# Kernel optimization log

Measured on AMD Instinct MI355X. Metric: run time of the kernel, lower is better.

Reference implementation:

```python
import jax, jax.numpy as jnp
from jax import lax
import numpy as np

ALPHA = 0.5
MAX_ITERS = 40
TOL = 1e-6
BITS = 8


def fake_quant_sym(w, bits=BITS):
    # symmetric per-tensor fake quantisation
    qmax = float(2 ** (bits - 1) - 1)
    scale = jnp.max(jnp.abs(w)) / qmax
    return jnp.round(w / scale) * scale


def fb_solve(Wq, Uq, bq, x, alpha=ALPHA, max_iters=MAX_ITERS, tol=TOL):
    # forward-backward splitting fixed-point solve: z = relu((1-a)z + a(Wz + Ux^T + b))
    n = Wq.shape[0]
    B = x.shape[0]
    Ux = Uq @ x.T + bq[:, None]  # (n, B), constant across iterations

    def cond(carry):
        z, res, it = carry
        return jnp.logical_and(it < max_iters, res >= tol)

    def body(carry):
        z, _, it = carry
        u = (1.0 - alpha) * z + alpha * (Wq @ z + Ux)
        z_next = jax.nn.relu(u)  # relu_prox
        res = jnp.linalg.norm(z_next - z) / (jnp.linalg.norm(z) + 1e-12)
        return z_next, res, it + 1

    z0 = jnp.zeros((n, B), dtype=x.dtype)
    z, _, _ = lax.while_loop(cond, body, (z0, jnp.array(jnp.inf, dtype=x.dtype), 0))
    u_star = (1.0 - alpha) * z + alpha * (Wq @ z + Ux)
    mask = (u_star > 0).astype(x.dtype)  # relu Jacobian mask D*
    return z, mask


def setup_inputs() -> dict:
    key = jax.random.key(0)
    k0, k1, k2, k3, k4 = jax.random.split(key, 5)
    n, d, B, C = 512, 784, 128, 10
    # scale W so ||W||_2 < 1 (monotone operator condition m > 0)
    W = 0.3 * jax.random.normal(k0, (n, n), dtype=jnp.float32) / jnp.sqrt(n)
    U = jax.random.normal(k1, (n, d), dtype=jnp.float32) / jnp.sqrt(d)
    b = 0.01 * jax.random.normal(k2, (n,), dtype=jnp.float32)
    x = jax.random.normal(k3, (B, d), dtype=jnp.float32)
    Wc = jax.random.normal(k4, (C, n), dtype=jnp.float32) / jnp.sqrt(n)
    bc = jnp.zeros((C,), dtype=jnp.float32)
    return {"W": W, "U": U, "b": b, "x": x, "Wc": Wc, "bc": bc}


def reference(W, U, b, x, Wc, bc):
    # post-training fake quantisation of W, U, b (done once at init in torch)
    Wq = fake_quant_sym(W)
    Uq = fake_quant_sym(U)
    bq = fake_quant_sym(b)
    z_star, _ = fb_solve(Wq, Uq, bq, x)  # (n, B)
    logits = z_star.T @ Wc.T + bc  # classifier on z*^T
    return logits
```

## Files before the change

### kernel.cpp

```cpp
#include <hip/hip_runtime.h>
#include <hip/hip_bf16.h>


#define N_DIM 512
#define D_DIM 784
#define B_DIM 128
#define C_DIM 10
#define QMAX 127.0f
#define N_ITERS 40
#define HILO_START 28
#define ZPITCH 528
#define UXPITCH 520
#define MT 4

typedef int    i32x4  __attribute__((ext_vector_type(4)));
typedef float  f32x4  __attribute__((ext_vector_type(4)));
typedef __bf16 bf16x8 __attribute__((ext_vector_type(8)));

__device__ __forceinline__ float pscale64(const float* __restrict__ p) {
    float m = 0.0f;
#pragma unroll 16
    for (int i = 0; i < 64; ++i) m = fmaxf(m, p[i]);
    return m * (1.0f / QMAX);
}

__global__ void maxabs_kernel(const float* __restrict__ W,
                              const float* __restrict__ U,
                              const float* __restrict__ b,
                              float* __restrict__ partials) {
    const float4* src;
    int n4;
    if (blockIdx.y == 0)      { src = (const float4*)W; n4 = N_DIM * N_DIM / 4; }
    else if (blockIdx.y == 1) { src = (const float4*)U; n4 = N_DIM * D_DIM / 4; }
    else                      { src = (const float4*)b; n4 = N_DIM / 4; }
    float m = 0.0f;
    for (int i = blockIdx.x * blockDim.x + threadIdx.x; i < n4; i += gridDim.x * blockDim.x) {
        float4 v = src[i];
        m = fmaxf(m, fmaxf(fmaxf(fabsf(v.x), fabsf(v.y)), fmaxf(fabsf(v.z), fabsf(v.w))));
    }
    __shared__ float red[256];
    red[threadIdx.x] = m;
    __syncthreads();
    for (int s = 128; s > 0; s >>= 1) {
        if (threadIdx.x < s) red[threadIdx.x] = fmaxf(red[threadIdx.x], red[threadIdx.x + s]);
        __syncthreads();
    }
    if (threadIdx.x == 0) partials[blockIdx.y * 64 + blockIdx.x] = red[0];
}

__global__ __launch_bounds__(256) void prep_kernel(const float* __restrict__ W,
                                                   const float* __restrict__ U,
                                                   const float* __restrict__ b,
                                                   const float* __restrict__ x,
                                                   const float* __restrict__ partials,
                                                   int* __restrict__ rowsum,
                                                   signed char* __restrict__ Qp8,
                                                   float* __restrict__ UxT) {
    const int t = threadIdx.x;
    if (blockIdx.x < 256) {
        __shared__ int ls[4];
        const float s = pscale64(partials);
        const float inv = 1.0f / s;
        int idx = blockIdx.x * 256 + t;
        float4 w = ((const float4*)W)[idx];
        int k = (idx << 2) & (N_DIM - 1);
        int r = (idx << 2) >> 9;
        int q0 = (int)rintf(w.x * inv);
        int q1 = (int)rintf(w.y * inv);
        int q2 = (int)rintf(w.z * inv);
        int q3 = (int)rintf(w.w * inv);
        char4 c;
        c.x = (signed char)q0; c.y = (signed char)q1;
        c.z = (signed char)q2; c.w = (signed char)q3;
        int kc = k >> 6, q = (k >> 4) & 3, jj = k & 15;
        *(char4*)&Qp8[((kc << 9) + r) * 64 + q * 16 + jj] = c;
        int psum = q0 + q1 + q2 + q3;
#pragma unroll
        for (int s2 = 1; s2 < 64; s2 <<= 1) psum += __shfl_xor(psum, s2);
        if ((t & 63) == 0) ls[t >> 6] = psum;
        __syncthreads();
        if (t == 0) {
            rowsum[2 * blockIdx.x]     = ls[0] + ls[1];
            rowsum[2 * blockIdx.x + 1] = ls[2] + ls[3];
        }
    } else {
        const float sU = pscale64(partials + 64);
        const float invU = 1.0f / sU;
        const float sb = pscale64(partials + 128);
        const int bx = blockIdx.x - 256;
        const int wave = t >> 6, lane = t & 63;
        const int m = lane & 15, quad = lane >> 4;
        const int i0 = (bx >> 3) * 64 + wave * 16;
        const int c0 = (bx & 7) * 16;
        const float* urow = U + (i0 + m) * D_DIM;
        const float* xrow = x + (c0 + m) * D_DIM;
        f32x4 acc = {};
#pragma unroll 4
        for (int kcc = 0; kcc < 24; ++kcc) {
            int kbase = kcc * 32 + (quad << 3);
            float4 u0 = *(const float4*)(urow + kbase);
            float4 u1 = *(const float4*)(urow + kbase + 4);
            float4 x0 = *(const float4*)(xrow + kbase);
            float4 x1 = *(const float4*)(xrow + kbase + 4);
            float uu[8] = {u0.x, u0.y, u0.z, u0.w, u1.x, u1.y, u1.z, u1.w};
            float xx[8] = {x0.x, x0.y, x0.z, x0.w, x1.x, x1.y, x1.z, x1.w};
            bf16x8 a, xh, xl;
#pragma unroll
            for (int j = 0; j < 8; ++j) {
                a[j] = (__bf16)rintf(uu[j] * invU);
                __bf16 h = (__bf16)xx[j];
                xh[j] = h;
                xl[j] = (__bf16)(xx[j] - (float)h);
            }
            acc = __builtin_amdgcn_mfma_f32_16x16x32_bf16(a, xh, acc, 0, 0, 0);
            acc = __builtin_amdgcn_mfma_f32_16x16x32_bf16(a, xl, acc, 0, 0, 0);
        }
        {
            bf16x8 a, xh, xl;
            if (quad < 2) {
                int kbase = 768 + (quad << 3);
                float4 u0 = *(const float4*)(urow + kbase);
                float4 u1 = *(const float4*)(urow + kbase + 4);
                float4 x0 = *(const float4*)(xrow + kbase);
                float4 x1 = *(const float4*)(xrow + kbase + 4);
                float uu[8] = {u0.x, u0.y, u0.z, u0.w, u1.x, u1.y, u1.z, u1.w};
                float xx[8] = {x0.x, x0.y, x0.z, x0.w, x1.x, x1.y, x1.z, x1.w};
#pragma unroll
                for (int j = 0; j < 8; ++j) {
                    a[j] = (__bf16)rintf(uu[j] * invU);
                    __bf16 h = (__bf16)xx[j];
                    xh[j] = h;
                    xl[j] = (__bf16)(xx[j] - (float)h);
                }
            } else {
#pragma unroll
                for (int j = 0; j < 8; ++j) {
                    a[j] = (__bf16)0.0f; xh[j] = (__bf16)0.0f; xl[j] = (__bf16)0.0f;
                }
            }
            acc = __builtin_amdgcn_mfma_f32_16x16x32_bf16(a, xh, acc, 0, 0, 0);
            acc = __builtin_amdgcn_mfma_f32_16x16x32_bf16(a, xl, acc, 0, 0, 0);
        }
        const int row0 = i0 + (quad << 2);
        f32x4 o;
#pragma unroll
        for (int r = 0; r < 4; ++r)
            o[r] = sU * acc[r] + rintf(b[row0 + r] / sb) * sb;
        *(f32x4*)&UxT[(c0 + m) * N_DIM + row0] = o;
    }
}

__global__ __launch_bounds__(512, 2) void solve_kernel(const signed char* __restrict__ Qp8,
                                                       const float* __restrict__ UxT,
                                                       const float* __restrict__ partials,
                                                       const int* __restrict__ rowsum,
                                                       const float* __restrict__ Wc,
                                                       const float* __restrict__ bc,
                                                       float* __restrict__ out) {
    __shared__ signed char zh[2][16][ZPITCH];
    __shared__ signed char zl[2][16][ZPITCH];
    __shared__ float UxS[16][UXPITCH];
    __shared__ float red[32][16][C_DIM];
    const int t = threadIdx.x;
    const int wave = t >> 6;
    const int lane = t & 63;
    const int m = lane & 15;
    const int quad = lane >> 4;
    const int c0 = blockIdx.x * 16;
    const float sW = pscale64(partials);
    const float c1 = sW * (1.0f / 2048.0f);

    for (int i = t; i < 16 * N_DIM; i += 512) {
        int c = i >> 9, r = i & (N_DIM - 1);
        float v = UxT[(c0 + c) * N_DIM + r];
        float z1 = fmaxf(0.5f * v, 0.0f);
        int vq = (int)rintf(z1 * 2048.0f);
        vq = min(vq, 32767);
        zh[0][c][r] = (signed char)(vq >> 8);
        zl[0][c][r] = (signed char)((vq & 255) - 128);
        UxS[c][r] = v + c1 * 128.0f * (float)rowsum[r];
    }

    const int rowbase = wave * 64;
    i32x4 A[MT][8];
#pragma unroll
    for (int ti = 0; ti < MT; ++ti)
#pragma unroll
        for (int kc = 0; kc < 8; ++kc)
            A[ti][kc] = *(const i32x4*)&Qp8[((kc << 9) + rowbase + ti * 16 + m) * 64 + (quad << 4)];
#pragma unroll
    for (int ti = 0; ti < MT; ++ti)
#pragma unroll
        for (int kc = 0; kc < 8; ++kc)
            asm volatile("" : "+v"(A[ti][kc]));
    __syncthreads();

    int cur = 0;
    for (int it = 1; it < N_ITERS; ++it) {
        const bool lo = (it >= HILO_START);
        i32x4 acch[MT] = {};
        i32x4 accl[MT] = {};
        if (lo) {
#pragma unroll
            for (int kc = 0; kc < 8; ++kc) {
                i32x4 bh = *(const i32x4*)&zh[cur][m][(kc << 6) + (quad << 4)];
                i32x4 bl = *(const i32x4*)&zl[cur][m][(kc << 6) + (quad << 4)];
#pragma unroll
                for (int ti = 0; ti < MT; ++ti) {
                    acch[ti] = __builtin_amdgcn_mfma_i32_16x16x64_i8(A[ti][kc], bh, acch[ti], 0, 0, 0);
                    accl[ti] = __builtin_amdgcn_mfma_i32_16x16x64_i8(A[ti][kc], bl, accl[ti], 0, 0, 0);
                }
            }
        } else {
#pragma unroll
            for (int kc = 0; kc < 8; ++kc) {
                i32x4 bh = *(const i32x4*)&zh[cur][m][(kc << 6) + (quad << 4)];
#pragma unroll
                for (int ti = 0; ti < MT; ++ti)
                    acch[ti] = __builtin_amdgcn_mfma_i32_16x16x64_i8(A[ti][kc], bh, acch[ti], 0, 0, 0);
            }
        }
        const int nxt = cur ^ 1;
#pragma unroll
        for (int ti = 0; ti < MT; ++ti) {
            const int row0 = rowbase + ti * 16 + (quad << 2);
            f32x4 uxv = *(const f32x4*)&UxS[m][row0];
            char4 ph = *(const char4*)&zh[cur][m][row0];
            char4 pl = *(const char4*)&zl[cur][m][row0];
            char4 nh, nl;
#pragma unroll
            for (int r = 0; r < 4; ++r) {
                int vp = (((int)((&ph.x)[r])) << 8) + (int)((&pl.x)[r]) + 128;
                int qv = (acch[ti][r] << 8) + (lo ? accl[ti][r] : 0);
                float u = 0.5f * ((float)vp * (1.0f / 2048.0f))
                        + 0.5f * (c1 * (float)qv + uxv[r]);
                float zn = fmaxf(u, 0.0f);
                int vq = (int)rintf(zn * 2048.0f);
                vq = min(vq, 32767);
                (&nh.x)[r] = (signed char)(vq >> 8);
                (&nl.x)[r] = (signed char)((vq & 255) - 128);
            }
            *(char4*)&zh[nxt][m][row0] = nh;
            *(char4*)&zl[nxt][m][row0] = nl;
        }
        __syncthreads();
        cur = nxt;
    }

    {
        const int seg = t >> 4;
        const int colL = t & 15;
        float p[C_DIM];
#pragma unroll
        for (int cl = 0; cl < C_DIM; ++cl) p[cl] = 0.0f;
        const int r0 = seg * 16;
#pragma unroll
        for (int rr = 0; rr < 16; ++rr) {
            int r = r0 + rr;
            int v = (((int)zh[cur][colL][r]) << 8) + (int)zl[cur][colL][r] + 128;
            float zv = (float)v * (1.0f / 2048.0f);
#pragma unroll
            for (int cl = 0; cl < C_DIM; ++cl)
                p[cl] += zv * Wc[cl * N_DIM + r];
        }
#pragma unroll
        for (int cl = 0; cl < C_DIM; ++cl) red[seg][colL][cl] = p[cl];
        __syncthreads();
        for (int s = 16; s > 0; s >>= 1) {
            if (seg < s) {
#pragma unroll
                for (int cl = 0; cl < C_DIM; ++cl)
                    red[seg][colL][cl] += red[seg + s][colL][cl];
            }
            __syncthreads();
        }
        if (t < 16 * C_DIM) {
            int col = t & 15;
            int cl  = t >> 4;
            out[(c0 + col) * C_DIM + cl] = red[0][col][cl] + bc[cl];
        }
    }
}

extern "C" void kernel_launch(void* const* d_in, const int* in_sizes, int n_in,
                              void* d_out, int out_size, void* d_ws, size_t ws_size,
                              hipStream_t stream) {
    const float* W  = (const float*)d_in[0];
    const float* U  = (const float*)d_in[1];
    const float* b  = (const float*)d_in[2];
    const float* x  = (const float*)d_in[3];
    const float* Wc = (const float*)d_in[4];
    const float* bc = (const float*)d_in[5];
    float* out = (float*)d_out;

    float* ws = (float*)d_ws;
    float* partials = ws;
    int* rowsum = (int*)(ws + 256);
    signed char* Qp8 = (signed char*)(ws + 256 + 512);
    float* UxT = ws + 256 + 512 + (N_DIM * N_DIM / 4);

    maxabs_kernel<<<dim3(64, 3), 256, 0, stream>>>(W, U, b, partials);
    prep_kernel<<<320, 256, 0, stream>>>(W, U, b, x, partials, rowsum, Qp8, UxT);
    solve_kernel<<<8, 512, 0, stream>>>(Qp8, UxT, partials, rowsum, Wc, bc, out);
}
```

Measured before the change: 166.1 us.

## Keep iterate z and Ux in registers; restage Ux GEMM through LDS

Result: faster. 158.3 us (-4.7%).

```diff
diff --git a/kernel.cpp b/kernel.cpp
--- a/kernel.cpp
+++ b/kernel.cpp
@@ -10,8 +10,8 @@
 #define N_ITERS 40
 #define HILO_START 28
 #define ZPITCH 528
-#define UXPITCH 520
 #define MT 4
+#define UPITCH 808
 
 typedef int    i32x4  __attribute__((ext_vector_type(4)));
 typedef float  f32x4  __attribute__((ext_vector_type(4)));
@@ -56,9 +56,13 @@
                                                    int* __restrict__ rowsum,
                                                    signed char* __restrict__ Qp8,
                                                    float* __restrict__ UxT) {
+    __shared__ __bf16 uS[16][UPITCH];
+    __shared__ __bf16 xhS[16][UPITCH];
+    __shared__ __bf16 xlS[16][UPITCH];
+    __shared__ f32x4  sacc[4][64];
+    __shared__ int ls[4];
     const int t = threadIdx.x;
     if (blockIdx.x < 256) {
-        __shared__ int ls[4];
         const float s = pscale64(partials);
         const float inv = 1.0f / s;
         int idx = blockIdx.x * 256 + t;
@@ -88,65 +92,46 @@
         const float invU = 1.0f / sU;
         const float sb = pscale64(partials + 128);
         const int bx = blockIdx.x - 256;
+        const int i0 = (bx >> 3) * 16;
+        const int c0 = (bx & 7) * 16;
+        for (int r = 0; r < 16; ++r) {
+            for (int k = t; k < D_DIM; k += 256) {
+                float uv = U[(i0 + r) * D_DIM + k];
+                uS[r][k] = (__bf16)rintf(uv * invU);
+                float xv = x[(c0 + r) * D_DIM + k];
+                __bf16 h = (__bf16)xv;
+                xhS[r][k] = h;
+                xlS[r][k] = (__bf16)(xv - (float)h);
+            }
+        }
+        for (int i = t; i < 16 * 16; i += 256) {
+            int r = i >> 4, k = D_DIM + (i & 15);
+            uS[r][k] = (__bf16)0.0f; xhS[r][k] = (__bf16)0.0f; xlS[r][k] = (__bf16)0.0f;
+        }
+        __syncthreads();
         const int wave = t >> 6, lane = t & 63;
         const int m = lane & 15, quad = lane >> 4;
-        const int i0 = (bx >> 3) * 64 + wave * 16;
-        const int c0 = (bx & 7) * 16;
-        const float* urow = U + (i0 + m) * D_DIM;
-        const float* xrow = x + (c0 + m) * D_DIM;
         f32x4 acc = {};
-#pragma unroll 4
-        for (int kcc = 0; kcc < 24; ++kcc) {
-            int kbase = kcc * 32 + (quad << 3);
-            float4 u0 = *(const float4*)(urow + kbase);
-            float4 u1 = *(const float4*)(urow + kbase + 4);
-            float4 x0 = *(const float4*)(xrow + kbase);
-            float4 x1 = *(const float4*)(xrow + kbase + 4);
-            float uu[8] = {u0.x, u0.y, u0.z, u0.w, u1.x, u1.y, u1.z, u1.w};
-            float xx[8] = {x0.x, x0.y, x0.z, x0.w, x1.x, x1.y, x1.z, x1.w};
-            bf16x8 a, xh, xl;
-#pragma unroll
-            for (int j = 0; j < 8; ++j) {
-                a[j] = (__bf16)rintf(uu[j] * invU);
-                __bf16 h = (__bf16)xx[j];
-                xh[j] = h;
-                xl[j] = (__bf16)(xx[j] - (float)h);
-            }
-            acc = __builtin_amdgcn_mfma_f32_16x16x32_bf16(a, xh, acc, 0, 0, 0);
-            acc = __builtin_amdgcn_mfma_f32_16x16x32_bf16(a, xl, acc, 0, 0, 0);
-        }
-        {
-            bf16x8 a, xh, xl;
-            if (quad < 2) {
-                int kbase = 768 + (quad << 3);
-                float4 u0 = *(const float4*)(urow + kbase);
-                float4 u1 = *(const float4*)(urow + kbase + 4);
-                float4 x0 = *(const float4*)(xrow + kbase);
-                float4 x1 = *(const float4*)(xrow + kbase + 4);
-                float uu[8] = {u0.x, u0.y, u0.z, u0.w, u1.x, u1.y, u1.z, u1.w};
-                float xx[8] = {x0.x, x0.y, x0.z, x0.w, x1.x, x1.y, x1.z, x1.w};
-#pragma unroll
-                for (int j = 0; j < 8; ++j) {
-                    a[j] = (__bf16)rintf(uu[j] * invU);
-                    __bf16 h = (__bf16)xx[j];
-                    xh[j] = h;
-                    xl[j] = (__bf16)(xx[j] - (float)h);
-                }
-            } else {
-#pragma unroll
-                for (int j = 0; j < 8; ++j) {
-                    a[j] = (__bf16)0.0f; xh[j] = (__bf16)0.0f; xl[j] = (__bf16)0.0f;
-                }
-            }
-            acc = __builtin_amdgcn_mfma_f32_16x16x32_bf16(a, xh, acc, 0, 0, 0);
-            acc = __builtin_amdgcn_mfma_f32_16x16x32_bf16(a, xl, acc, 0, 0, 0);
-        }
-        const int row0 = i0 + (quad << 2);
-        f32x4 o;
-#pragma unroll
-        for (int r = 0; r < 4; ++r)
-            o[r] = sU * acc[r] + rintf(b[row0 + r] / sb) * sb;
-        *(f32x4*)&UxT[(c0 + m) * N_DIM + row0] = o;
+        for (int kc = wave; kc < 25; kc += 4) {
+            bf16x8 a  = *(const bf16x8*)&uS[m][kc * 32 + (quad << 3)];
+            bf16x8 bh = *(const bf16x8*)&xhS[m][kc * 32 + (quad << 3)];
+            bf16x8 bl = *(const bf16x8*)&xlS[m][kc * 32 + (quad << 3)];
+            acc = __builtin_amdgcn_mfma_f32_16x16x32_bf16(a, bh, acc, 0, 0, 0);
+            acc = __builtin_amdgcn_mfma_f32_16x16x32_bf16(a, bl, acc, 0, 0, 0);
+        }
+        sacc[wave][lane] = acc;
+        __syncthreads();
+        if (wave == 0) {
+            f32x4 s0 = sacc[0][lane], s1 = sacc[1][lane];
+            f32x4 s2 = sacc[2][lane], s3 = sacc[3][lane];
+            const int row0 = i0 + (quad << 2);
+            f32x4 o;
+#pragma unroll
+            for (int r = 0; r < 4; ++r)
+                o[r] = sU * (s0[r] + s1[r] + s2[r] + s3[r])
+                     + rintf(b[row0 + r] / sb) * sb;
+            *(f32x4*)&UxT[(c0 + m) * N_DIM + row0] = o;
+        }
     }
 }
 
@@ -159,7 +144,6 @@
                                                        float* __restrict__ out) {
     __shared__ signed char zh[2][16][ZPITCH];
     __shared__ signed char zl[2][16][ZPITCH];
-    __shared__ float UxS[16][UXPITCH];
     __shared__ float red[32][16][C_DIM];
     const int t = threadIdx.x;
     const int wave = t >> 6;
@@ -169,19 +153,32 @@
     const int c0 = blockIdx.x * 16;
     const float sW = pscale64(partials);
     const float c1 = sW * (1.0f / 2048.0f);
-
-    for (int i = t; i < 16 * N_DIM; i += 512) {
-        int c = i >> 9, r = i & (N_DIM - 1);
-        float v = UxT[(c0 + c) * N_DIM + r];
-        float z1 = fmaxf(0.5f * v, 0.0f);
-        int vq = (int)rintf(z1 * 2048.0f);
-        vq = min(vq, 32767);
-        zh[0][c][r] = (signed char)(vq >> 8);
-        zl[0][c][r] = (signed char)((vq & 255) - 128);
-        UxS[c][r] = v + c1 * 128.0f * (float)rowsum[r];
-    }
+    const float hc_hi = c1 * 128.0f;
+    const float hc_lo = c1 * 0.5f;
 
     const int rowbase = wave * 64;
+    float zreg[MT][4];
+    float uxh[MT][4];
+#pragma unroll
+    for (int ti = 0; ti < MT; ++ti) {
+        const int row0 = rowbase + ti * 16 + (quad << 2);
+        int vq[4];
+#pragma unroll
+        for (int r = 0; r < 4; ++r) {
+            float v = UxT[(c0 + m) * N_DIM + row0 + r];
+            uxh[ti][r] = 0.5f * (v + c1 * 128.0f * (float)rowsum[row0 + r]);
+            float z1 = fmaxf(0.5f * v, 0.0f);
+            zreg[ti][r] = z1;
+            vq[r] = min((int)rintf(z1 * 2048.0f), 32767);
+        }
+        unsigned int h = (unsigned int)(vq[0] >> 8) | ((unsigned int)(vq[1] >> 8) << 8)
+                       | ((unsigned int)(vq[2] >> 8) << 16) | ((unsigned int)(vq[3] >> 8) << 24);
+        unsigned int l = (unsigned int)(vq[0] & 255) | ((unsigned int)(vq[1] & 255) << 8)
+                       | ((unsigned int)(vq[2] & 255) << 16) | ((unsigned int)(vq[3] & 255) << 24);
+        *(unsigned int*)&zh[0][m][row0] = h;
+        *(unsigned int*)&zl[0][m][row0] = l ^ 0x80808080u;
+    }
+
     i32x4 A[MT][8];
 #pragma unroll
     for (int ti = 0; ti < MT; ++ti)
@@ -198,6 +195,7 @@
     int cur = 0;
     for (int it = 1; it < N_ITERS; ++it) {
         const bool lo = (it >= HILO_START);
+        const bool wlo = (it >= HILO_START - 1);
         i32x4 acch[MT] = {};
         i32x4 accl[MT] = {};
         if (lo) {
@@ -224,53 +222,53 @@
 #pragma unroll
         for (int ti = 0; ti < MT; ++ti) {
             const int row0 = rowbase + ti * 16 + (quad << 2);
-            f32x4 uxv = *(const f32x4*)&UxS[m][row0];
-            char4 ph = *(const char4*)&zh[cur][m][row0];
-            char4 pl = *(const char4*)&zl[cur][m][row0];
-            char4 nh, nl;
+            int vq[4];
 #pragma unroll
             for (int r = 0; r < 4; ++r) {
-                int vp = (((int)((&ph.x)[r])) << 8) + (int)((&pl.x)[r]) + 128;
-                int qv = (acch[ti][r] << 8) + (lo ? accl[ti][r] : 0);
-                float u = 0.5f * ((float)vp * (1.0f / 2048.0f))
-                        + 0.5f * (c1 * (float)qv + uxv[r]);
+                float base = fmaf(0.5f, zreg[ti][r], uxh[ti][r]);
+                float u = lo ? fmaf(hc_hi, (float)acch[ti][r], fmaf(hc_lo, (float)accl[ti][r], base))
+                             : fmaf(hc_hi, (float)acch[ti][r], base);
                 float zn = fmaxf(u, 0.0f);
-                int vq = (int)rintf(zn * 2048.0f);
-                vq = min(vq, 32767);
-                (&nh.x)[r] = (signed char)(vq >> 8);
-                (&nl.x)[r] = (signed char)((vq & 255) - 128);
-            }
-            *(char4*)&zh[nxt][m][row0] = nh;
-            *(char4*)&zl[nxt][m][row0] = nl;
+                zreg[ti][r] = zn;
+                vq[r] = min((int)rintf(zn * 2048.0f), 32767);
+            }
+            unsigned int h = (unsigned int)(vq[0] >> 8) | ((unsigned int)(vq[1] >> 8) << 8)
+                           | ((unsigned int)(vq[2] >> 8) << 16) | ((unsigned int)(vq[3] >> 8) << 24);
+            *(unsigned int*)&zh[nxt][m][row0] = h;
+            if (wlo) {
+                unsigned int l = (unsigned int)(vq[0] & 255) | ((unsigned int)(vq[1] & 255) << 8)
+                               | ((unsigned int)(vq[2] & 255) << 16) | ((unsigned int)(vq[3] & 255) << 24);
+                *(unsigned int*)&zl[nxt][m][row0] = l ^ 0x80808080u;
+            }
         }
         __syncthreads();
         cur = nxt;
     }
 
     {
-        const int seg = t >> 4;
-        const int colL = t & 15;
+        const int grp = wave * 4 + quad;
         float p[C_DIM];
 #pragma unroll
         for (int cl = 0; cl < C_DIM; ++cl) p[cl] = 0.0f;
-        const int r0 = seg * 16;
-#pragma unroll
-        for (int rr = 0; rr < 16; ++rr) {
-            int r = r0 + rr;
-            int v = (((int)zh[cur][colL][r]) << 8) + (int)zl[cur][colL][r] + 128;
-            float zv = (float)v * (1.0f / 2048.0f);
-#pragma unroll
-            for (int cl = 0; cl < C_DIM; ++cl)
-                p[cl] += zv * Wc[cl * N_DIM + r];
-        }
-#pragma unroll
-        for (int cl = 0; cl < C_DIM; ++cl) red[seg][colL][cl] = p[cl];
+#pragma unroll
+        for (int ti = 0; ti < MT; ++ti) {
+            const int row0 = rowbase + ti * 16 + (quad << 2);
+#pragma unroll
+            for (int r = 0; r < 4; ++r) {
+                float zv = zreg[ti][r];
+#pragma unroll
+                for (int cl = 0; cl < C_DIM; ++cl)
+                    p[cl] += zv * Wc[cl * N_DIM + row0 + r];
+            }
+        }
+#pragma unroll
+        for (int cl = 0; cl < C_DIM; ++cl) red[grp][m][cl] = p[cl];
         __syncthreads();
         for (int s = 16; s > 0; s >>= 1) {
-            if (seg < s) {
+            if (grp < s) {
 #pragma unroll
                 for (int cl = 0; cl < C_DIM; ++cl)
-                    red[seg][colL][cl] += red[seg + s][colL][cl];
+                    red[grp][m][cl] += red[grp + s][m][cl];
             }
             __syncthreads();
         }
@@ -300,6 +298,6 @@
     float* UxT = ws + 256 + 512 + (N_DIM * N_DIM / 4);
 
     maxabs_kernel<<<dim3(64, 3), 256, 0, stream>>>(W, U, b, partials);
-    prep_kernel<<<320, 256, 0, stream>>>(W, U, b, x, partials, rowsum, Qp8, UxT);
+    prep_kernel<<<512, 256, 0, stream>>>(W, U, b, x, partials, rowsum, Qp8, UxT);
     solve_kernel<<<8, 512, 0, stream>>>(Qp8, UxT, partials, rowsum, Wc, bc, out);
 }
```
